# Kernel tuning notes

Hardware: AMD Instinct MI355X
Metric: run time of the kernel (lower is better)

The kernel has to match this reference:

```python
import jax, jax.numpy as jnp
import numpy as np

BATCH = 4096
DIM = 128
TEMP = 0.5
EPS = 1e-8


def _neg_mask(batch):
    n = 2 * batch
    m = np.ones((n, n), dtype=bool)
    np.fill_diagonal(m, False)
    idx = np.arange(batch)
    m[idx, idx + batch] = False
    m[idx + batch, idx] = False
    return m


def setup_inputs() -> dict:
    key = jax.random.key(0)
    k1, k2 = jax.random.split(key)
    zx = jax.random.normal(k1, (BATCH, DIM), dtype=jnp.float32)
    zy = jax.random.normal(k2, (BATCH, DIM), dtype=jnp.float32)
    return {"zx": zx, "zy": zy}


def reference(zx, zy):
    batch = zx.shape[0]
    n = 2 * batch  # N = 2 * batch_size
    z = jnp.concatenate([zx, zy], axis=0)  # [N, D]
    # cosine similarity = normalized GEMM (avoids O(N^2*D) intermediate)
    norm = jnp.maximum(jnp.linalg.norm(z, axis=1, keepdims=True), EPS)
    zn = z / norm
    sim = (zn @ zn.T) / TEMP  # [N, N]
    # positives: diagonals at offsets +batch and -batch
    sim_xy = jnp.diagonal(sim, offset=batch)
    sim_yx = jnp.diagonal(sim, offset=-batch)
    positives = jnp.concatenate([sim_xy, sim_yx]).reshape(n, 1)  # [N, 1]
    # negatives: mask out diagonal and positive pairs (static boolean mask)
    mask = _neg_mask(batch)
    negatives = sim[mask].reshape(n, n - 2)  # [N, N-2]
    logits = jnp.concatenate([positives, negatives], axis=1)  # [N, N-1]
    # CrossEntropy(labels=0, reduction='sum') / N
    loss = jnp.sum(jax.nn.logsumexp(logits, axis=1) - logits[:, 0]) / n
    return loss
```

## Files before the change

kernel.cpp:

```cpp
#include <hip/hip_runtime.h>
#include <hip/hip_bf16.h>

#define BATCH 4096
#define NROWS 8192
#define DIM   128

typedef __bf16 bf16x8 __attribute__((ext_vector_type(8)));
typedef __bf16 bf16x2 __attribute__((ext_vector_type(2)));
typedef float  f32x4  __attribute__((ext_vector_type(4)));

typedef const __attribute__((address_space(1))) unsigned int* gptr_t;
typedef __attribute__((address_space(3))) unsigned int* lptr_t;

__global__ __launch_bounds__(256) void normalize_kernel(
    const float* __restrict__ zx, const float* __restrict__ zy,
    ushort* __restrict__ zn)
{
  const int tid  = threadIdx.x;
  const int lane = tid & 63;
  const int w    = tid >> 6;
  const int row  = blockIdx.x * 4 + w;
  const float* src = (row < BATCH) ? (zx + (size_t)row * DIM)
                                   : (zy + (size_t)(row - BATCH) * DIM);
  float2 v = ((const float2*)src)[lane];
  float ss = v.x * v.x + v.y * v.y;
#pragma unroll
  for (int off = 1; off < 64; off <<= 1)
    ss += __shfl_xor(ss, off, 64);
  float inv = 1.0f / fmaxf(sqrtf(ss), 1e-8f);
  bf16x2 st;
  st.x = (__bf16)(v.x * inv);
  st.y = (__bf16)(v.y * inv);
  reinterpret_cast<bf16x2*>(zn + (size_t)row * DIM)[lane] = st;
}

__global__ __launch_bounds__(256, 2) void simloss_kernel(
    const ushort* __restrict__ zn, float* __restrict__ S, float* __restrict__ P)
{
  __shared__ ushort Bs[128 * 128];
  const int tid  = threadIdx.x;
  const int lane = tid & 63;
  const int w    = tid >> 6;
  const int wr   = w >> 1, wc = w & 1;
  const int rb    = blockIdx.x;
  const int strip = blockIdx.y;
  const int q    = lane >> 4;
  const int l15  = lane & 15;

  bf16x8 af[4][4];
  {
    const int arow = rb * 128 + wr * 64 + l15;
#pragma unroll
    for (int mi = 0; mi < 4; ++mi)
#pragma unroll
      for (int ks = 0; ks < 4; ++ks) {
        const ushort* ap = zn + (size_t)(arow + mi * 16) * DIM + ks * 32 + q * 8;
        af[mi][ks] = *reinterpret_cast<const bf16x8*>(ap);
      }
  }

  float Srow[4][4];
#pragma unroll
  for (int mi = 0; mi < 4; ++mi)
#pragma unroll
    for (int r = 0; r < 4; ++r) Srow[mi][r] = 0.f;

  const float K1 = 2.8853900817779268f;

  for (int it = 0; it < 8; ++it) {
    const int ct = strip * 8 + it;
    const int C0 = ct * 128;

    __syncthreads();
#pragma unroll
    for (int j = 0; j < 8; ++j) {
      const int Lbase = w * 512 + j * 64;
      const int row   = w * 32 + j * 4 + q;
      const int c     = l15 ^ (row & 15);
      const ushort* g = zn + (size_t)(C0 + row) * DIM + c * 8;
      __builtin_amdgcn_global_load_lds((gptr_t)g, (lptr_t)(Bs + Lbase * 8), 16, 0, 0);
    }
    __syncthreads();

    f32x4 acc[4][4];
#pragma unroll
    for (int mi = 0; mi < 4; ++mi)
#pragma unroll
      for (int ni = 0; ni < 4; ++ni)
        acc[mi][ni] = (f32x4){0.f, 0.f, 0.f, 0.f};

#pragma unroll
    for (int ks = 0; ks < 4; ++ks) {
      bf16x8 bf[4];
#pragma unroll
      for (int ni = 0; ni < 4; ++ni) {
        const int nl  = wc * 64 + ni * 16 + l15;
        const int ck  = ks * 4 + q;
        const int L   = nl * 16 + (ck ^ (nl & 15));
        bf[ni] = *reinterpret_cast<const bf16x8*>(Bs + L * 8);
      }
#pragma unroll
      for (int mi = 0; mi < 4; ++mi)
#pragma unroll
        for (int ni = 0; ni < 4; ++ni)
          acc[mi][ni] = __builtin_amdgcn_mfma_f32_16x16x32_bf16(
              af[mi][ks], bf[ni], acc[mi][ni], 0, 0, 0);
    }

    const bool diag = (ct == rb);
    const bool part = (ct == (rb ^ 32));
#pragma unroll
    for (int mi = 0; mi < 4; ++mi)
#pragma unroll
      for (int ni = 0; ni < 4; ++ni)
#pragma unroll
        for (int r = 0; r < 4; ++r) {
          float d = acc[mi][ni][r];
          float v = __builtin_amdgcn_exp2f(fmaf(d, K1, -K1));
          if (diag) {
            const int rl = wr * 64 + mi * 16 + q * 4 + r;
            const int cl = wc * 64 + ni * 16 + l15;
            if (rl == cl) v = 0.f;
          }
          Srow[mi][r] += v;
        }

    if (part) {
#pragma unroll
      for (int mi = 0; mi < 4; ++mi) {
        const int rl0 = wr * 64 + mi * 16 + q * 4;
#pragma unroll
        for (int ni = 0; ni < 4; ++ni) {
          const int cl = wc * 64 + ni * 16 + l15;
#pragma unroll
          for (int r = 0; r < 4; ++r) {
            if (cl == rl0 + r)
              P[rb * 128 + rl0 + r] = 2.0f * acc[mi][ni][r];
          }
        }
      }
    }
  }

#pragma unroll
  for (int mi = 0; mi < 4; ++mi)
#pragma unroll
    for (int r = 0; r < 4; ++r) {
      float v = Srow[mi][r];
      v += __shfl_xor(v, 1, 64);
      v += __shfl_xor(v, 2, 64);
      v += __shfl_xor(v, 4, 64);
      v += __shfl_xor(v, 8, 64);
      if (l15 == 0)
        atomicAdd(&S[rb * 128 + wr * 64 + mi * 16 + q * 4 + r], v);
    }
}

__global__ __launch_bounds__(256) void finalize_kernel(
    const float* __restrict__ S, const float* __restrict__ P,
    float* __restrict__ out)
{
  const int i = blockIdx.x * 256 + threadIdx.x;
  float c = 2.0f + logf(S[i]) - P[i];
#pragma unroll
  for (int off = 1; off < 64; off <<= 1)
    c += __shfl_xor(c, off, 64);
  __shared__ float wsum[4];
  const int lane = threadIdx.x & 63, w = threadIdx.x >> 6;
  if (lane == 0) wsum[w] = c;
  __syncthreads();
  if (threadIdx.x == 0)
    atomicAdd(out, (wsum[0] + wsum[1] + wsum[2] + wsum[3]) * (1.0f / NROWS));
}

extern "C" void kernel_launch(void* const* d_in, const int* in_sizes, int n_in,
                              void* d_out, int out_size, void* d_ws, size_t ws_size,
                              hipStream_t stream)
{
  const float* zx = (const float*)d_in[0];
  const float* zy = (const float*)d_in[1];
  ushort* zn = (ushort*)d_ws;
  float*  S  = (float*)((char*)d_ws + (size_t)NROWS * DIM * 2);
  float*  P  = S + NROWS;
  float*  out = (float*)d_out;

  hipMemsetAsync(S, 0, NROWS * sizeof(float), stream);
  hipMemsetAsync(out, 0, sizeof(float), stream);
  normalize_kernel<<<NROWS / 4, 256, 0, stream>>>(zx, zy, zn);
  simloss_kernel<<<dim3(64, 8), 256, 0, stream>>>(zn, S, P);
  finalize_kernel<<<NROWS / 256, 256, 0, stream>>>(S, P, out);
}
```

Baseline: 87.40 us.

## Exploit similarity symmetry with upper-triangular tiles and drop memsets

The similarity kernel now launches one block per upper-triangular 128x128 tile (2080 tiles) instead of computing the full matrix. Each off-diagonal tile adds its exp sums to both its row and column accumulators, which roughly halves the MFMA and exp work. LDS staging is removed and operands are read straight from global memory. The two memsets are folded into the normalize kernel and a single-block finalize writes the output, cutting launch overhead, at the cost of more atomics and uncoalesced global fragment loads.

```diff
diff --git a/kernel.cpp b/kernel.cpp
--- a/kernel.cpp
+++ b/kernel.cpp
@@ -9,12 +9,9 @@
 typedef __bf16 bf16x2 __attribute__((ext_vector_type(2)));
 typedef float  f32x4  __attribute__((ext_vector_type(4)));
 
-typedef const __attribute__((address_space(1))) unsigned int* gptr_t;
-typedef __attribute__((address_space(3))) unsigned int* lptr_t;
-
 __global__ __launch_bounds__(256) void normalize_kernel(
     const float* __restrict__ zx, const float* __restrict__ zy,
-    ushort* __restrict__ zn)
+    ushort* __restrict__ zn, float* __restrict__ S)
 {
   const int tid  = threadIdx.x;
   const int lane = tid & 63;
@@ -32,115 +29,85 @@
   st.x = (__bf16)(v.x * inv);
   st.y = (__bf16)(v.y * inv);
   reinterpret_cast<bf16x2*>(zn + (size_t)row * DIM)[lane] = st;
+  if (lane == 0) S[row] = 0.f;
 }
 
-__global__ __launch_bounds__(256, 2) void simloss_kernel(
+__global__ __launch_bounds__(256) void simloss_kernel(
     const ushort* __restrict__ zn, float* __restrict__ S, float* __restrict__ P)
 {
-  __shared__ ushort Bs[128 * 128];
   const int tid  = threadIdx.x;
   const int lane = tid & 63;
   const int w    = tid >> 6;
   const int wr   = w >> 1, wc = w & 1;
-  const int rb    = blockIdx.x;
-  const int strip = blockIdx.y;
   const int q    = lane >> 4;
   const int l15  = lane & 15;
 
-  bf16x8 af[4][4];
-  {
-    const int arow = rb * 128 + wr * 64 + l15;
+  const int t = blockIdx.x;
+  int rb = (int)(0.5f * (129.0f - sqrtf((float)(16641 - 8 * t))));
+  while (rb * (129 - rb) / 2 > t) --rb;
+  while ((rb + 1) * (128 - rb) / 2 <= t) ++rb;
+  const int cb = rb + (t - rb * (129 - rb) / 2);
+
+  const int R0 = rb * 128, C0 = cb * 128;
+  const int abase = (R0 + wr * 64 + l15) * DIM + q * 8;
+  const int bbase = (C0 + wc * 64 + l15) * DIM + q * 8;
+
+  f32x4 acc[4][4];
+#pragma unroll
+  for (int mi = 0; mi < 4; ++mi)
+#pragma unroll
+    for (int ni = 0; ni < 4; ++ni)
+      acc[mi][ni] = (f32x4){0.f, 0.f, 0.f, 0.f};
+
+#pragma unroll
+  for (int ks = 0; ks < 4; ++ks) {
+    bf16x8 af[4], bf[4];
+#pragma unroll
+    for (int mi = 0; mi < 4; ++mi)
+      af[mi] = *reinterpret_cast<const bf16x8*>(zn + abase + mi * 16 * DIM + ks * 32);
+#pragma unroll
+    for (int ni = 0; ni < 4; ++ni)
+      bf[ni] = *reinterpret_cast<const bf16x8*>(zn + bbase + ni * 16 * DIM + ks * 32);
 #pragma unroll
     for (int mi = 0; mi < 4; ++mi)
 #pragma unroll
-      for (int ks = 0; ks < 4; ++ks) {
-        const ushort* ap = zn + (size_t)(arow + mi * 16) * DIM + ks * 32 + q * 8;
-        af[mi][ks] = *reinterpret_cast<const bf16x8*>(ap);
-      }
+      for (int ni = 0; ni < 4; ++ni)
+        acc[mi][ni] = __builtin_amdgcn_mfma_f32_16x16x32_bf16(
+            af[mi], bf[ni], acc[mi][ni], 0, 0, 0);
   }
 
+  const float K1 = 2.8853900817779268f;
+  const bool diag = (rb == cb);
+  const bool part = (cb == rb + 32);
+
   float Srow[4][4];
+  float Scol[4];
 #pragma unroll
   for (int mi = 0; mi < 4; ++mi)
 #pragma unroll
     for (int r = 0; r < 4; ++r) Srow[mi][r] = 0.f;
-
-  const float K1 = 2.8853900817779268f;
-
-  for (int it = 0; it < 8; ++it) {
-    const int ct = strip * 8 + it;
-    const int C0 = ct * 128;
-
-    __syncthreads();
 #pragma unroll
-    for (int j = 0; j < 8; ++j) {
-      const int Lbase = w * 512 + j * 64;
-      const int row   = w * 32 + j * 4 + q;
-      const int c     = l15 ^ (row & 15);
-      const ushort* g = zn + (size_t)(C0 + row) * DIM + c * 8;
-      __builtin_amdgcn_global_load_lds((gptr_t)g, (lptr_t)(Bs + Lbase * 8), 16, 0, 0);
-    }
-    __syncthreads();
-
-    f32x4 acc[4][4];
-#pragma unroll
-    for (int mi = 0; mi < 4; ++mi)
-#pragma unroll
-      for (int ni = 0; ni < 4; ++ni)
-        acc[mi][ni] = (f32x4){0.f, 0.f, 0.f, 0.f};
+  for (int ni = 0; ni < 4; ++ni) Scol[ni] = 0.f;
 
 #pragma unroll
-    for (int ks = 0; ks < 4; ++ks) {
-      bf16x8 bf[4];
+  for (int mi = 0; mi < 4; ++mi)
 #pragma unroll
-      for (int ni = 0; ni < 4; ++ni) {
-        const int nl  = wc * 64 + ni * 16 + l15;
-        const int ck  = ks * 4 + q;
-        const int L   = nl * 16 + (ck ^ (nl & 15));
-        bf[ni] = *reinterpret_cast<const bf16x8*>(Bs + L * 8);
-      }
+    for (int ni = 0; ni < 4; ++ni)
 #pragma unroll
-      for (int mi = 0; mi < 4; ++mi)
-#pragma unroll
-        for (int ni = 0; ni < 4; ++ni)
-          acc[mi][ni] = __builtin_amdgcn_mfma_f32_16x16x32_bf16(
-              af[mi][ks], bf[ni], acc[mi][ni], 0, 0, 0);
-    }
-
-    const bool diag = (ct == rb);
-    const bool part = (ct == (rb ^ 32));
-#pragma unroll
-    for (int mi = 0; mi < 4; ++mi)
-#pragma unroll
-      for (int ni = 0; ni < 4; ++ni)
-#pragma unroll
-        for (int r = 0; r < 4; ++r) {
-          float d = acc[mi][ni][r];
-          float v = __builtin_amdgcn_exp2f(fmaf(d, K1, -K1));
-          if (diag) {
-            const int rl = wr * 64 + mi * 16 + q * 4 + r;
-            const int cl = wc * 64 + ni * 16 + l15;
-            if (rl == cl) v = 0.f;
-          }
-          Srow[mi][r] += v;
-        }
-
-    if (part) {
-#pragma unroll
-      for (int mi = 0; mi < 4; ++mi) {
-        const int rl0 = wr * 64 + mi * 16 + q * 4;
-#pragma unroll
-        for (int ni = 0; ni < 4; ++ni) {
-          const int cl = wc * 64 + ni * 16 + l15;
-#pragma unroll
-          for (int r = 0; r < 4; ++r) {
-            if (cl == rl0 + r)
-              P[rb * 128 + rl0 + r] = 2.0f * acc[mi][ni][r];
-          }
+      for (int r = 0; r < 4; ++r) {
+        const float d = acc[mi][ni][r];
+        float v = __builtin_amdgcn_exp2f(fmaf(d, K1, -K1));
+        const int rl = wr * 64 + mi * 16 + q * 4 + r;
+        const int cl = wc * 64 + ni * 16 + l15;
+        if (diag && rl == cl) v = 0.f;
+        Srow[mi][r] += v;
+        Scol[ni] += v;
+        if (part && rl == cl) {
+          const float p = 2.0f * d;
+          P[R0 + rl] = p;
+          P[C0 + cl] = p;
         }
       }
-    }
-  }
 
 #pragma unroll
   for (int mi = 0; mi < 4; ++mi)
@@ -152,25 +119,41 @@
       v += __shfl_xor(v, 4, 64);
       v += __shfl_xor(v, 8, 64);
       if (l15 == 0)
-        atomicAdd(&S[rb * 128 + wr * 64 + mi * 16 + q * 4 + r], v);
+        atomicAdd(&S[R0 + wr * 64 + mi * 16 + q * 4 + r], v);
     }
+
+  if (!diag) {
+#pragma unroll
+    for (int ni = 0; ni < 4; ++ni) {
+      float v = Scol[ni];
+      v += __shfl_xor(v, 16, 64);
+      v += __shfl_xor(v, 32, 64);
+      if (q == 0)
+        atomicAdd(&S[C0 + wc * 64 + ni * 16 + l15], v);
+    }
+  }
 }
 
-__global__ __launch_bounds__(256) void finalize_kernel(
+__global__ __launch_bounds__(1024) void finalize_kernel(
     const float* __restrict__ S, const float* __restrict__ P,
     float* __restrict__ out)
 {
-  const int i = blockIdx.x * 256 + threadIdx.x;
-  float c = 2.0f + logf(S[i]) - P[i];
+  float c = 0.f;
+  for (int i = threadIdx.x; i < NROWS; i += 1024)
+    c += 2.0f + logf(S[i]) - P[i];
 #pragma unroll
   for (int off = 1; off < 64; off <<= 1)
     c += __shfl_xor(c, off, 64);
-  __shared__ float wsum[4];
+  __shared__ float wsum[16];
   const int lane = threadIdx.x & 63, w = threadIdx.x >> 6;
   if (lane == 0) wsum[w] = c;
   __syncthreads();
-  if (threadIdx.x == 0)
-    atomicAdd(out, (wsum[0] + wsum[1] + wsum[2] + wsum[3]) * (1.0f / NROWS));
+  if (threadIdx.x == 0) {
+    float s = 0.f;
+#pragma unroll
+    for (int k = 0; k < 16; ++k) s += wsum[k];
+    out[0] = s * (1.0f / NROWS);
+  }
 }
 
 extern "C" void kernel_launch(void* const* d_in, const int* in_sizes, int n_in,
@@ -184,9 +167,7 @@
   float*  P  = S + NROWS;
   float*  out = (float*)d_out;
 
-  hipMemsetAsync(S, 0, NROWS * sizeof(float), stream);
-  hipMemsetAsync(out, 0, sizeof(float), stream);
-  normalize_kernel<<<NROWS / 4, 256, 0, stream>>>(zx, zy, zn);
-  simloss_kernel<<<dim3(64, 8), 256, 0, stream>>>(zn, S, P);
-  finalize_kernel<<<NROWS / 256, 256, 0, stream>>>(S, P, out);
+  normalize_kernel<<<NROWS / 4, 256, 0, stream>>>(zx, zy, zn, S);
+  simloss_kernel<<<2080, 256, 0, stream>>>(zn, S, P);
+  finalize_kernel<<<1, 1024, 0, stream>>>(S, P, out);
 }
```

Result: slower. 114.9 us (+31.5%).
